# Performance work log

Measured on AMD Instinct MI355X. Metric: run time of the kernel, lower is better.

Reference implementation:

```python
import jax, jax.numpy as jnp
import numpy as np

N = 100_000      # nodes
E = 1_600_000    # edges (avg degree 16)
IN, H, OUT = 960, 192, 3
NB = 6           # block_num


def setup_inputs() -> dict:
    key = jax.random.key(0)
    ks = jax.random.split(key, 14)
    s = 0.05  # weight init scale
    x = jax.random.normal(ks[0], (N, IN), jnp.float32)
    src = jax.random.randint(ks[1], (E,), 0, N, jnp.int32)
    dst = jax.random.randint(ks[2], (E,), 0, N, jnp.int32)
    # normalized adjacency values (like D^-1 A entries)
    ew = jax.random.uniform(ks[3], (E,), jnp.float32) / 16.0
    w1 = jax.random.normal(ks[4], (IN, H), jnp.float32) * s
    l1 = jax.random.normal(ks[5], (IN, H), jnp.float32) * s
    b1 = jnp.zeros((H,), jnp.float32)
    wb = jax.random.normal(ks[6], (2 * NB, H, H), jnp.float32) * s
    lb = jax.random.normal(ks[7], (2 * NB, H, H), jnp.float32) * s
    bb = jnp.zeros((2 * NB, H), jnp.float32)
    w2 = jax.random.normal(ks[8], (H, OUT), jnp.float32) * s
    l2 = jax.random.normal(ks[9], (H, OUT), jnp.float32) * s
    b2 = jnp.zeros((OUT,), jnp.float32)
    return dict(x=x, src=src, dst=dst, ew=ew, w1=w1, l1=l1, b1=b1,
                wb=wb, lb=lb, bb=bb, w2=w2, l2=l2, b2=b2)


def reference(x, src, dst, ew, w1, l1, b1, wb, lb, bb, w2, l2, b2):
    def gcn(h, w, lw, b):
        # GraphConvolution: spmm(adj, h @ w) + h @ loop_w + b
        sup = h @ w                                   # [N, F_out]
        msg = sup[src] * ew[:, None]                  # gather + weight  [E, F_out]
        agg = jax.ops.segment_sum(msg, dst, num_segments=N)
        return agg + h @ lw + b

    h = gcn(x, w1, l1, b1)                            # conv1: in_dim -> hidden
    for i in range(NB):                               # GResBlocks
        a = gcn(h, wb[2 * i], lb[2 * i], bb[2 * i])
        a = gcn(a, wb[2 * i + 1], lb[2 * i + 1], bb[2 * i + 1])
        h = (h + a) * 0.5                             # residual scaling
    x_cat = h
    x_out = gcn(x_cat, w2, l2, b2)                    # conv2: hidden -> out_dim
    return (x_out, x_cat)
```

## Files before the change

### kernel.cpp

```cpp
#include <hip/hip_runtime.h>

typedef __attribute__((ext_vector_type(8))) short short8;
typedef __attribute__((ext_vector_type(4))) float f32x4;
typedef __attribute__((ext_vector_type(4))) int int4v;
typedef __attribute__((ext_vector_type(2))) unsigned int u32x2;

__device__ __forceinline__ float bf2f(unsigned short u) {
  return __uint_as_float(((unsigned)u) << 16);
}
__device__ __forceinline__ unsigned short f2bf(float f) {
  unsigned u = __float_as_uint(f);
  return (unsigned short)((u + 0x7FFFu + ((u >> 16) & 1u)) >> 16);
}

#define GLB_CAST(p) ((const __attribute__((address_space(1))) void*)(p))
#define LDS_CAST(p) ((__attribute__((address_space(3))) void*)(p))

__global__ void count_kernel(const int* __restrict__ dst, int* __restrict__ cnt, int E) {
  int e = blockIdx.x * blockDim.x + threadIdx.x;
  if (e < E) atomicAdd(&cnt[dst[e] + 1], 1);
}

__global__ __launch_bounds__(256) void scan_bsum_kernel(const int* __restrict__ cnt,
                                                        int* __restrict__ bsum, int n) {
  __shared__ int buf[256];
  int tid = threadIdx.x;
  int j0 = blockIdx.x * 1024 + tid * 4;
  int s = 0;
#pragma unroll
  for (int k = 0; k < 4; k++) {
    int j = j0 + k;
    if (j < n) s += cnt[j];
  }
  buf[tid] = s;
  __syncthreads();
  for (int off = 128; off > 0; off >>= 1) {
    if (tid < off) buf[tid] += buf[tid + off];
    __syncthreads();
  }
  if (tid == 0) bsum[blockIdx.x] = buf[0];
}

__global__ __launch_bounds__(256) void scan_small_kernel(const int* __restrict__ bsum,
                                                         int* __restrict__ boff, int nb) {
  __shared__ int buf[2][256];
  int tid = threadIdx.x;
  int C = (nb + 255) >> 8;
  int start = tid * C;
  int end = start + C; if (end > nb) end = nb;
  int s = 0;
  for (int j = start; j < end; j++) s += bsum[j];
  buf[0][tid] = s;
  __syncthreads();
  int pin = 0;
  for (int off = 1; off < 256; off <<= 1) {
    int v = buf[pin][tid];
    if (tid >= off) v += buf[pin][tid - off];
    buf[pin ^ 1][tid] = v;
    pin ^= 1;
    __syncthreads();
  }
  int run = (tid == 0) ? 0 : buf[pin][tid - 1];
  for (int j = start; j < end; j++) {
    boff[j] = run;
    run += bsum[j];
  }
}

__global__ __launch_bounds__(256) void scan_final_kernel(const int* __restrict__ cnt,
                                                         const int* __restrict__ boff,
                                                         int* __restrict__ rowptr,
                                                         int* __restrict__ cur,
                                                         int n, int nrows) {
  __shared__ int buf[2][256];
  int tid = threadIdx.x;
  int j0 = blockIdx.x * 1024 + tid * 4;
  int v[4];
  int s = 0;
#pragma unroll
  for (int k = 0; k < 4; k++) {
    int j = j0 + k;
    v[k] = (j < n) ? cnt[j] : 0;
    s += v[k];
  }
  buf[0][tid] = s;
  __syncthreads();
  int pin = 0;
  for (int off = 1; off < 256; off <<= 1) {
    int t = buf[pin][tid];
    if (tid >= off) t += buf[pin][tid - off];
    buf[pin ^ 1][tid] = t;
    pin ^= 1;
    __syncthreads();
  }
  int run = boff[blockIdx.x] + ((tid == 0) ? 0 : buf[pin][tid - 1]);
#pragma unroll
  for (int k = 0; k < 4; k++) {
    int j = j0 + k;
    if (j < n) {
      run += v[k];
      rowptr[j] = run;
      if (j < nrows) cur[j] = run;
    }
  }
}

__global__ void fill_kernel(const int* __restrict__ src, const int* __restrict__ dst,
                            const float* __restrict__ ew,
                            int* __restrict__ cur, int2* __restrict__ s_edge, int E) {
  int e = blockIdx.x * blockDim.x + threadIdx.x;
  if (e >= E) return;
  int r = dst[e];
  int pos = atomicAdd(&cur[r], 1);
  s_edge[pos] = make_int2(src[e], __float_as_int(ew[e]));
}

__global__ void prep_w_kernel(const float* __restrict__ w1,
                              const float* __restrict__ l1,
                              const float* __restrict__ wb,
                              const float* __restrict__ lb,
                              unsigned short* __restrict__ Wt1,
                              unsigned short* __restrict__ Wtb) {
  int tid = blockIdx.x * blockDim.x + threadIdx.x;
  const int n1 = 384 * 960;
  const int nb = 12 * 384 * 192;
  if (tid < n1) {
    int c = tid / 960, k = tid % 960;
    Wt1[tid] = f2bf((c < 192) ? w1[k * 192 + c] : l1[k * 192 + (c - 192)]);
  } else if (tid < n1 + nb) {
    int u = tid - n1;
    int i = u / (384 * 192);
    int r = u % (384 * 192);
    int c = r / 192, k = r % 192;
    Wtb[u] = f2bf((c < 192) ? wb[(i * 192 + k) * 192 + c]
                            : lb[(i * 192 + k) * 192 + (c - 192)]);
  }
}

__device__ __forceinline__ short8 cvt_f32x8(const float* p) {
  f32x4 a = *reinterpret_cast<const f32x4*>(p);
  f32x4 b = *reinterpret_cast<const f32x4*>(p + 4);
  short8 r;
  r[0] = (short)f2bf(a[0]); r[1] = (short)f2bf(a[1]);
  r[2] = (short)f2bf(a[2]); r[3] = (short)f2bf(a[3]);
  r[4] = (short)f2bf(b[0]); r[5] = (short)f2bf(b[1]);
  r[6] = (short)f2bf(b[2]); r[7] = (short)f2bf(b[3]);
  return r;
}

template <typename T>
__global__ __launch_bounds__(512) void gemm_kernel(const T* __restrict__ A,
                                                   const unsigned short* __restrict__ Wt,
                                                   unsigned short* __restrict__ out,
                                                   int nrows, int K) {
  __shared__ char lds_raw[40960];

  int tid = threadIdx.x;
  int lane = tid & 63;
  int w = tid >> 6;
  int rg = w >> 1, ch = w & 1;
  int row0blk = blockIdx.x * 256;
  int row0 = row0blk + rg * 64;
  int l15 = lane & 15, lq = lane >> 4;

  f32x4 acc[12][4];
#pragma unroll
  for (int cf = 0; cf < 12; cf++)
#pragma unroll
    for (int rf = 0; rf < 4; rf++) acc[cf][rf] = (f32x4)(0.0f);

  int tiles = K / 32;
  for (int tile = 0; tile < tiles; ++tile) {
    __syncthreads();
#pragma unroll
    for (int it = 0; it < 3; ++it) {
      int slot = it * 512 + tid;
      int q = slot / 384, c = slot - q * 384;
      const unsigned short* g = Wt + (size_t)c * K + tile * 32 + q * 8;
      __builtin_amdgcn_global_load_lds(GLB_CAST(g), LDS_CAST(lds_raw + 16384 + slot * 16), 16, 0, 0);
    }
#pragma unroll
    for (int it = 0; it < 2; ++it) {
      int slot = it * 512 + tid;
      int c = slot >> 8, row = slot & 255;
      int grow = row0blk + row;
      if (grow > nrows - 1) grow = nrows - 1;
      if constexpr (sizeof(T) == 2) {
        const T* g = A + (size_t)grow * K + tile * 32 + c * 8;
        __builtin_amdgcn_global_load_lds(GLB_CAST(g), LDS_CAST(lds_raw + slot * 16), 16, 0, 0);
      } else {
        const float* g = (const float*)A + (size_t)grow * K + tile * 32 + c * 8;
        *reinterpret_cast<short8*>(lds_raw + slot * 16) = cvt_f32x8(g);
      }
    }
    __syncthreads();

    short8 af[4];
#pragma unroll
    for (int rf = 0; rf < 4; rf++)
      af[rf] = *reinterpret_cast<const short8*>(
          lds_raw + lq * 4096 + (rg * 64 + rf * 16 + l15) * 16);
#pragma unroll
    for (int cf = 0; cf < 12; cf++) {
      const short8 bf = *reinterpret_cast<const short8*>(
          lds_raw + 16384 + (lq * 384 + ch * 192 + cf * 16 + l15) * 16);
#pragma unroll
      for (int rf = 0; rf < 4; rf++)
        acc[cf][rf] = __builtin_amdgcn_mfma_f32_16x16x32_bf16(bf, af[rf], acc[cf][rf], 0, 0, 0);
    }
  }

#pragma unroll
  for (int rf = 0; rf < 4; rf++) {
    int row = row0 + rf * 16 + l15;
    if (row >= nrows) continue;
    unsigned short* orow = out + (size_t)row * 384 + ch * 192 + lq * 4;
#pragma unroll
    for (int cf = 0; cf < 12; cf++) {
      u32x2 pv;
      pv[0] = (unsigned)f2bf(acc[cf][rf][0]) | ((unsigned)f2bf(acc[cf][rf][1]) << 16);
      pv[1] = (unsigned)f2bf(acc[cf][rf][2]) | ((unsigned)f2bf(acc[cf][rf][3]) << 16);
      *reinterpret_cast<u32x2*>(orow + cf * 16) = pv;
    }
  }
}

__global__ __launch_bounds__(256) void spmm_kernel(const unsigned short* __restrict__ t,
                                                   const int* __restrict__ rowptr,
                                                   const int2* __restrict__ s_edge,
                                                   const float* __restrict__ bias,
                                                   const float* __restrict__ hprev32,
                                                   unsigned short* __restrict__ out16,
                                                   float* __restrict__ out32,
                                                   int n, int mode) {
  int tid = blockIdx.x * blockDim.x + threadIdx.x;
  int node = tid / 24;
  int c = tid % 24;
  if (node >= n) return;

  float acc[8];
#pragma unroll
  for (int j = 0; j < 8; j++) acc[j] = 0.0f;

  int e0 = rowptr[node], e1 = rowptr[node + 1];
  int e = e0;
  for (; e + 4 <= e1; e += 4) {
    int2 ra = s_edge[e];
    int2 rb = s_edge[e + 1];
    int2 rc = s_edge[e + 2];
    int2 rd = s_edge[e + 3];
    float wa = __int_as_float(ra.y), wb = __int_as_float(rb.y);
    float wc = __int_as_float(rc.y), wd = __int_as_float(rd.y);
    short8 va = *reinterpret_cast<const short8*>(&t[(size_t)ra.x * 384 + c * 8]);
    short8 vb = *reinterpret_cast<const short8*>(&t[(size_t)rb.x * 384 + c * 8]);
    short8 vc = *reinterpret_cast<const short8*>(&t[(size_t)rc.x * 384 + c * 8]);
    short8 vd = *reinterpret_cast<const short8*>(&t[(size_t)rd.x * 384 + c * 8]);
#pragma unroll
    for (int j = 0; j < 8; j++) {
      acc[j] += wa * bf2f((unsigned short)va[j]) + wb * bf2f((unsigned short)vb[j]) +
                wc * bf2f((unsigned short)vc[j]) + wd * bf2f((unsigned short)vd[j]);
    }
  }
  for (; e < e1; e++) {
    int2 ra = s_edge[e];
    float wa = __int_as_float(ra.y);
    short8 va = *reinterpret_cast<const short8*>(&t[(size_t)ra.x * 384 + c * 8]);
#pragma unroll
    for (int j = 0; j < 8; j++) acc[j] += wa * bf2f((unsigned short)va[j]);
  }

  short8 hlv = *reinterpret_cast<const short8*>(&t[(size_t)node * 384 + 192 + c * 8]);
  float r[8];
#pragma unroll
  for (int j = 0; j < 8; j++)
    r[j] = acc[j] + bf2f((unsigned short)hlv[j]) + bias[c * 8 + j];

  if (mode == 1) {
#pragma unroll
    for (int j = 0; j < 8; j++)
      r[j] = 0.5f * (hprev32[(size_t)node * 192 + c * 8 + j] + r[j]);
  }

  unsigned short o16[8];
#pragma unroll
  for (int j = 0; j < 8; j++) o16[j] = f2bf(r[j]);
  *reinterpret_cast<int4v*>(&out16[(size_t)node * 192 + c * 8]) =
      *reinterpret_cast<const int4v*>(o16);

  if (out32) {
    f32x4 lo, hi;
    lo[0] = r[0]; lo[1] = r[1]; lo[2] = r[2]; lo[3] = r[3];
    hi[0] = r[4]; hi[1] = r[5]; hi[2] = r[6]; hi[3] = r[7];
    *reinterpret_cast<f32x4*>(&out32[(size_t)node * 192 + c * 8]) = lo;
    *reinterpret_cast<f32x4*>(&out32[(size_t)node * 192 + c * 8 + 4]) = hi;
  }
}

__global__ __launch_bounds__(256) void conv2a_kernel(const float* __restrict__ h,
                                                     const float* __restrict__ w2,
                                                     const float* __restrict__ l2,
                                                     const float* __restrict__ b2,
                                                     float* __restrict__ sup2,
                                                     float* __restrict__ hl2, int n) {
  int wid = (blockIdx.x * blockDim.x + threadIdx.x) >> 6;
  int lane = threadIdx.x & 63;
  if (wid >= n) return;
  float sa[3] = {0.f, 0.f, 0.f}, sl[3] = {0.f, 0.f, 0.f};
  for (int k = lane; k < 192; k += 64) {
    float hv = h[(size_t)wid * 192 + k];
#pragma unroll
    for (int j = 0; j < 3; j++) {
      sa[j] += hv * w2[k * 3 + j];
      sl[j] += hv * l2[k * 3 + j];
    }
  }
#pragma unroll
  for (int j = 0; j < 3; j++) {
    for (int off = 32; off > 0; off >>= 1) {
      sa[j] += __shfl_down(sa[j], off);
      sl[j] += __shfl_down(sl[j], off);
    }
  }
  if (lane == 0) {
#pragma unroll
    for (int j = 0; j < 3; j++) {
      sup2[(size_t)wid * 3 + j] = sa[j];
      hl2[(size_t)wid * 3 + j] = sl[j] + b2[j];
    }
  }
}

__global__ __launch_bounds__(256) void conv2b_kernel(const int* __restrict__ rowptr,
                                                     const int2* __restrict__ s_edge,
                                                     const float* __restrict__ sup2,
                                                     const float* __restrict__ hl2,
                                                     float* __restrict__ out, int n) {
  int node = blockIdx.x * blockDim.x + threadIdx.x;
  if (node >= n) return;
  float acc[3] = {0.f, 0.f, 0.f};
  int e0 = rowptr[node], e1 = rowptr[node + 1];
  for (int e = e0; e < e1; e++) {
    int2 rec = s_edge[e];
    float wgt = __int_as_float(rec.y);
#pragma unroll
    for (int j = 0; j < 3; j++) acc[j] += wgt * sup2[(size_t)rec.x * 3 + j];
  }
#pragma unroll
  for (int j = 0; j < 3; j++)
    out[(size_t)node * 3 + j] = acc[j] + hl2[(size_t)node * 3 + j];
}

extern "C" void kernel_launch(void* const* d_in, const int* in_sizes, int n_in,
                              void* d_out, int out_size, void* d_ws, size_t ws_size,
                              hipStream_t stream) {
  const float* x  = (const float*)d_in[0];
  const int* src  = (const int*)d_in[1];
  const int* dst  = (const int*)d_in[2];
  const float* ew = (const float*)d_in[3];
  const float* w1 = (const float*)d_in[4];
  const float* l1 = (const float*)d_in[5];
  const float* b1 = (const float*)d_in[6];
  const float* wb = (const float*)d_in[7];
  const float* lb = (const float*)d_in[8];
  const float* bb = (const float*)d_in[9];
  const float* w2 = (const float*)d_in[10];
  const float* l2 = (const float*)d_in[11];
  const float* b2 = (const float*)d_in[12];
  float* out = (float*)d_out;

  const int N = in_sizes[0] / 960;
  const int E = in_sizes[1];

  float* h32 = out + (size_t)N * 3;

  char* p = (char*)d_ws;
  auto alloc = [&](size_t bytes) {
    char* q = p;
    p += (bytes + 255) & ~(size_t)255;
    return q;
  };
  unsigned short* Wt1 = (unsigned short*)alloc((size_t)384 * 960 * 2);
  unsigned short* Wtb = (unsigned short*)alloc((size_t)12 * 384 * 192 * 2);
  unsigned short* t   = (unsigned short*)alloc((size_t)N * 384 * 2);
  unsigned short* h16 = (unsigned short*)alloc((size_t)N * 192 * 2);
  unsigned short* a16 = (unsigned short*)alloc((size_t)N * 192 * 2);
  int* rowptr = (int*)alloc((size_t)(N + 1) * 4);
  int* cur    = (int*)alloc((size_t)N * 4);
  int* cnt    = (int*)alloc((size_t)(N + 1) * 4);
  int* bsum   = (int*)alloc((size_t)1024 * 4);
  int* boff   = (int*)alloc((size_t)1024 * 4);
  int2* s_edge = (int2*)alloc((size_t)E * 8);
  float* sup2 = (float*)alloc((size_t)N * 3 * 4);
  float* hl2  = (float*)alloc((size_t)N * 3 * 4);
  if ((size_t)(p - (char*)d_ws) > ws_size) return;

  const int nScan = N + 1;
  const int nBlk = (nScan + 1023) / 1024;

  hipMemsetAsync(cnt, 0, (size_t)(N + 1) * 4, stream);
  count_kernel<<<(E + 255) / 256, 256, 0, stream>>>(dst, cnt, E);
  scan_bsum_kernel<<<nBlk, 256, 0, stream>>>(cnt, bsum, nScan);
  scan_small_kernel<<<1, 256, 0, stream>>>(bsum, boff, nBlk);
  scan_final_kernel<<<nBlk, 256, 0, stream>>>(cnt, boff, rowptr, cur, nScan, N);
  fill_kernel<<<(E + 255) / 256, 256, 0, stream>>>(src, dst, ew, cur, s_edge, E);
  {
    int total = 384 * 960 + 12 * 384 * 192;
    prep_w_kernel<<<(total + 255) / 256, 256, 0, stream>>>(w1, l1, wb, lb, Wt1, Wtb);
  }

  int gBlocks = (N + 255) / 256;
  int sBlocks = (N * 24 + 255) / 256;

  gemm_kernel<float><<<gBlocks, 512, 0, stream>>>(x, Wt1, t, N, 960);
  spmm_kernel<<<sBlocks, 256, 0, stream>>>(t, rowptr, s_edge, b1,
                                           (const float*)nullptr, h16, h32, N, 0);

  for (int i = 0; i < 12; i += 2) {
    gemm_kernel<unsigned short><<<gBlocks, 512, 0, stream>>>(
        h16, Wtb + (size_t)i * 384 * 192, t, N, 192);
    spmm_kernel<<<sBlocks, 256, 0, stream>>>(t, rowptr, s_edge, bb + (size_t)i * 192,
                                             (const float*)nullptr, a16, (float*)nullptr, N, 0);
    gemm_kernel<unsigned short><<<gBlocks, 512, 0, stream>>>(
        a16, Wtb + (size_t)(i + 1) * 384 * 192, t, N, 192);
    spmm_kernel<<<sBlocks, 256, 0, stream>>>(t, rowptr, s_edge, bb + (size_t)(i + 1) * 192,
                                             h32, h16, h32, N, 1);
  }

  conv2a_kernel<<<(N + 3) / 4, 256, 0, stream>>>(h32, w2, l2, b2, sup2, hl2, N);
  conv2b_kernel<<<(N + 255) / 256, 256, 0, stream>>>(rowptr, s_edge, sup2, hl2, out, N);
}
```

Before: 2.569 ms.

## Double-buffer bf16 GEMM LDS staging and unroll SpMM gather to 8 edges

Splits the templated GEMM into an fp32-input kernel and a bf16 kernel that double-buffers its tiles in 80 KB of dynamic LDS. The next tile's global_load_lds is issued before the MFMA work on the current tile, so loads overlap compute and one barrier per tile is removed. The SpMM inner loop now gathers 8 neighbour rows per iteration instead of 4, giving more loads in flight. In exchange, the larger LDS footprint lowers how many GEMM blocks fit on a CU, and the longer SpMM unroll raises register pressure.

```diff
diff --git a/kernel.cpp b/kernel.cpp
--- a/kernel.cpp
+++ b/kernel.cpp
@@ -148,11 +148,10 @@
   return r;
 }
 
-template <typename T>
-__global__ __launch_bounds__(512) void gemm_kernel(const T* __restrict__ A,
-                                                   const unsigned short* __restrict__ Wt,
-                                                   unsigned short* __restrict__ out,
-                                                   int nrows, int K) {
+__global__ __launch_bounds__(512) void gemm_f32_kernel(const float* __restrict__ A,
+                                                       const unsigned short* __restrict__ Wt,
+                                                       unsigned short* __restrict__ out,
+                                                       int nrows, int K) {
   __shared__ char lds_raw[40960];
 
   int tid = threadIdx.x;
@@ -185,13 +184,8 @@
       int c = slot >> 8, row = slot & 255;
       int grow = row0blk + row;
       if (grow > nrows - 1) grow = nrows - 1;
-      if constexpr (sizeof(T) == 2) {
-        const T* g = A + (size_t)grow * K + tile * 32 + c * 8;
-        __builtin_amdgcn_global_load_lds(GLB_CAST(g), LDS_CAST(lds_raw + slot * 16), 16, 0, 0);
-      } else {
-        const float* g = (const float*)A + (size_t)grow * K + tile * 32 + c * 8;
-        *reinterpret_cast<short8*>(lds_raw + slot * 16) = cvt_f32x8(g);
-      }
+      const float* g = A + (size_t)grow * K + tile * 32 + c * 8;
+      *reinterpret_cast<short8*>(lds_raw + slot * 16) = cvt_f32x8(g);
     }
     __syncthreads();
 
@@ -208,6 +202,85 @@
       for (int rf = 0; rf < 4; rf++)
         acc[cf][rf] = __builtin_amdgcn_mfma_f32_16x16x32_bf16(bf, af[rf], acc[cf][rf], 0, 0, 0);
     }
+  }
+
+#pragma unroll
+  for (int rf = 0; rf < 4; rf++) {
+    int row = row0 + rf * 16 + l15;
+    if (row >= nrows) continue;
+    unsigned short* orow = out + (size_t)row * 384 + ch * 192 + lq * 4;
+#pragma unroll
+    for (int cf = 0; cf < 12; cf++) {
+      u32x2 pv;
+      pv[0] = (unsigned)f2bf(acc[cf][rf][0]) | ((unsigned)f2bf(acc[cf][rf][1]) << 16);
+      pv[1] = (unsigned)f2bf(acc[cf][rf][2]) | ((unsigned)f2bf(acc[cf][rf][3]) << 16);
+      *reinterpret_cast<u32x2*>(orow + cf * 16) = pv;
+    }
+  }
+}
+
+__global__ __launch_bounds__(512) void gemm_bf16_db_kernel(const unsigned short* __restrict__ A,
+                                                           const unsigned short* __restrict__ Wt,
+                                                           unsigned short* __restrict__ out,
+                                                           int nrows, int K) {
+  extern __shared__ char lds_db[];
+
+  int tid = threadIdx.x;
+  int lane = tid & 63;
+  int w = tid >> 6;
+  int rg = w >> 1, ch = w & 1;
+  int row0blk = blockIdx.x * 256;
+  int row0 = row0blk + rg * 64;
+  int l15 = lane & 15, lq = lane >> 4;
+
+  f32x4 acc[12][4];
+#pragma unroll
+  for (int cf = 0; cf < 12; cf++)
+#pragma unroll
+    for (int rf = 0; rf < 4; rf++) acc[cf][rf] = (f32x4)(0.0f);
+
+  auto stage = [&](int tile, int buf) {
+    char* base = lds_db + buf * 40960;
+#pragma unroll
+    for (int it = 0; it < 3; ++it) {
+      int slot = it * 512 + tid;
+      int q = slot / 384, c = slot - q * 384;
+      const unsigned short* g = Wt + (size_t)c * K + tile * 32 + q * 8;
+      __builtin_amdgcn_global_load_lds(GLB_CAST(g), LDS_CAST(base + 16384 + slot * 16), 16, 0, 0);
+    }
+#pragma unroll
+    for (int it = 0; it < 2; ++it) {
+      int slot = it * 512 + tid;
+      int c = slot >> 8, row = slot & 255;
+      int grow = row0blk + row;
+      if (grow > nrows - 1) grow = nrows - 1;
+      const unsigned short* g = A + (size_t)grow * K + tile * 32 + c * 8;
+      __builtin_amdgcn_global_load_lds(GLB_CAST(g), LDS_CAST(base + slot * 16), 16, 0, 0);
+    }
+  };
+
+  int tiles = K / 32;
+  stage(0, 0);
+  __syncthreads();
+  int cur = 0;
+  for (int tile = 0; tile < tiles; ++tile) {
+    if (tile + 1 < tiles) stage(tile + 1, cur ^ 1);
+    char* base = lds_db + cur * 40960;
+    short8 af[4];
+#pragma unroll
+    for (int rf = 0; rf < 4; rf++)
+      af[rf] = *reinterpret_cast<const short8*>(
+          base + lq * 4096 + (rg * 64 + rf * 16 + l15) * 16);
+#pragma unroll
+    for (int cf = 0; cf < 12; cf++) {
+      const short8 bf = *reinterpret_cast<const short8*>(
+          base + 16384 + (lq * 384 + ch * 192 + cf * 16 + l15) * 16);
+#pragma unroll
+      for (int rf = 0; rf < 4; rf++)
+        acc[cf][rf] = __builtin_amdgcn_mfma_f32_16x16x32_bf16(bf, af[rf], acc[cf][rf], 0, 0, 0);
+    }
+    __syncthreads();
+    cur ^= 1;
   }
 
 #pragma unroll
@@ -244,24 +317,32 @@
 
   int e0 = rowptr[node], e1 = rowptr[node + 1];
   int e = e0;
-  for (; e + 4 <= e1; e += 4) {
+  for (; e + 8 <= e1; e += 8) {
+    int2 rec[8];
+#pragma unroll
+    for (int k = 0; k < 8; k++) rec[k] = s_edge[e + k];
+    short8 v[8];
+#pragma unroll
+    for (int k = 0; k < 8; k++)
+      v[k] = *reinterpret_cast<const short8*>(&t[(size_t)rec[k].x * 384 + c * 8]);
+#pragma unroll
+    for (int k = 0; k < 8; k++) {
+      float wgt = __int_as_float(rec[k].y);
+#pragma unroll
+      for (int j = 0; j < 8; j++) acc[j] += wgt * bf2f((unsigned short)v[k][j]);
+    }
+  }
+  for (; e + 2 <= e1; e += 2) {
     int2 ra = s_edge[e];
     int2 rb = s_edge[e + 1];
-    int2 rc = s_edge[e + 2];
-    int2 rd = s_edge[e + 3];
     float wa = __int_as_float(ra.y), wb = __int_as_float(rb.y);
-    float wc = __int_as_float(rc.y), wd = __int_as_float(rd.y);
     short8 va = *reinterpret_cast<const short8*>(&t[(size_t)ra.x * 384 + c * 8]);
     short8 vb = *reinterpret_cast<const short8*>(&t[(size_t)rb.x * 384 + c * 8]);
-    short8 vc = *reinterpret_cast<const short8*>(&t[(size_t)rc.x * 384 + c * 8]);
-    short8 vd = *reinterpret_cast<const short8*>(&t[(size_t)rd.x * 384 + c * 8]);
-#pragma unroll
-    for (int j = 0; j < 8; j++) {
-      acc[j] += wa * bf2f((unsigned short)va[j]) + wb * bf2f((unsigned short)vb[j]) +
-                wc * bf2f((unsigned short)vc[j]) + wd * bf2f((unsigned short)vd[j]);
-    }
-  }
-  for (; e < e1; e++) {
+#pragma unroll
+    for (int j = 0; j < 8; j++)
+      acc[j] += wa * bf2f((unsigned short)va[j]) + wb * bf2f((unsigned short)vb[j]);
+  }
+  if (e < e1) {
     int2 ra = s_edge[e];
     float wa = __int_as_float(ra.y);
     short8 va = *reinterpret_cast<const short8*>(&t[(size_t)ra.x * 384 + c * 8]);
@@ -410,17 +491,18 @@
 
   int gBlocks = (N + 255) / 256;
   int sBlocks = (N * 24 + 255) / 256;
-
-  gemm_kernel<float><<<gBlocks, 512, 0, stream>>>(x, Wt1, t, N, 960);
+  const int DB_LDS = 81920;
+
+  gemm_f32_kernel<<<gBlocks, 512, 0, stream>>>(x, Wt1, t, N, 960);
   spmm_kernel<<<sBlocks, 256, 0, stream>>>(t, rowptr, s_edge, b1,
                                            (const float*)nullptr, h16, h32, N, 0);
 
   for (int i = 0; i < 12; i += 2) {
-    gemm_kernel<unsigned short><<<gBlocks, 512, 0, stream>>>(
+    gemm_bf16_db_kernel<<<gBlocks, 512, DB_LDS, stream>>>(
         h16, Wtb + (size_t)i * 384 * 192, t, N, 192);
     spmm_kernel<<<sBlocks, 256, 0, stream>>>(t, rowptr, s_edge, bb + (size_t)i * 192,
                                              (const float*)nullptr, a16, (float*)nullptr, N, 0);
-    gemm_kernel<unsigned short><<<gBlocks, 512, 0, stream>>>(
+    gemm_bf16_db_kernel<<<gBlocks, 512, DB_LDS, stream>>>(
         a16, Wtb + (size_t)(i + 1) * 384 * 192, t, N, 192);
     spmm_kernel<<<sBlocks, 256, 0, stream>>>(t, rowptr, s_edge, bb + (size_t)(i + 1) * 192,
                                              h32, h16, h32, N, 1);
```

After: 2.528 ms. About the same (-1.6%).

## Double-buffer GEMM LDS tiles with 128-row blocks and widen SpMM per-thread columns

Applied to the files above, without the earlier changes.

The GEMM kernel is rewritten to double-buffer LDS, prefetching the next K tile of A and weights while MFMAs run on the current one. The row tile shrinks from 256 to 128 rows per block, and the fp32 input conversion is deferred until after compute. The SpMM kernel now handles 16 columns per thread instead of 8, using 12 threads per node. The aim is to hide global-load latency in the GEMM and cut redundant edge-record loads in SpMM, at the cost of more registers and lower occupancy (64KB dynamic LDS per block).

```diff
diff --git a/kernel.cpp b/kernel.cpp
--- a/kernel.cpp
+++ b/kernel.cpp
@@ -137,9 +137,7 @@
   }
 }
 
-__device__ __forceinline__ short8 cvt_f32x8(const float* p) {
-  f32x4 a = *reinterpret_cast<const f32x4*>(p);
-  f32x4 b = *reinterpret_cast<const f32x4*>(p + 4);
+__device__ __forceinline__ short8 cvt_pair(f32x4 a, f32x4 b) {
   short8 r;
   r[0] = (short)f2bf(a[0]); r[1] = (short)f2bf(a[1]);
   r[2] = (short)f2bf(a[2]); r[3] = (short)f2bf(a[3]);
@@ -149,70 +147,96 @@
 }
 
 template <typename T>
-__global__ __launch_bounds__(512) void gemm_kernel(const T* __restrict__ A,
-                                                   const unsigned short* __restrict__ Wt,
-                                                   unsigned short* __restrict__ out,
-                                                   int nrows, int K) {
-  __shared__ char lds_raw[40960];
+__global__ __launch_bounds__(512) void gemm_db_kernel(const T* __restrict__ A,
+                                                      const unsigned short* __restrict__ Wt,
+                                                      unsigned short* __restrict__ out,
+                                                      int nrows, int K) {
+  extern __shared__ char lds[];
+  const int BUF = 32768;
 
   int tid = threadIdx.x;
   int lane = tid & 63;
   int w = tid >> 6;
   int rg = w >> 1, ch = w & 1;
-  int row0blk = blockIdx.x * 256;
-  int row0 = row0blk + rg * 64;
+  int row0blk = blockIdx.x * 128;
   int l15 = lane & 15, lq = lane >> 4;
 
-  f32x4 acc[12][4];
-#pragma unroll
-  for (int cf = 0; cf < 12; cf++)
-#pragma unroll
-    for (int rf = 0; rf < 4; rf++) acc[cf][rf] = (f32x4)(0.0f);
-
-  int tiles = K / 32;
-  for (int tile = 0; tile < tiles; ++tile) {
-    __syncthreads();
+  int skq = tid >> 7, srow = tid & 127;
+  int sgrow = row0blk + srow;
+  if (sgrow > nrows - 1) sgrow = nrows - 1;
+
+  f32x4 acc[12][2];
+#pragma unroll
+  for (int cf = 0; cf < 12; cf++) {
+    acc[cf][0] = (f32x4)(0.0f);
+    acc[cf][1] = (f32x4)(0.0f);
+  }
+
+  auto stageB = [&](int tile, int buf) {
 #pragma unroll
     for (int it = 0; it < 3; ++it) {
       int slot = it * 512 + tid;
       int q = slot / 384, c = slot - q * 384;
       const unsigned short* g = Wt + (size_t)c * K + tile * 32 + q * 8;
-      __builtin_amdgcn_global_load_lds(GLB_CAST(g), LDS_CAST(lds_raw + 16384 + slot * 16), 16, 0, 0);
-    }
-#pragma unroll
-    for (int it = 0; it < 2; ++it) {
-      int slot = it * 512 + tid;
-      int c = slot >> 8, row = slot & 255;
-      int grow = row0blk + row;
-      if (grow > nrows - 1) grow = nrows - 1;
+      __builtin_amdgcn_global_load_lds(GLB_CAST(g), LDS_CAST(lds + buf * BUF + 8192 + slot * 16),
+                                       16, 0, 0);
+    }
+  };
+
+  int tiles = K / 32;
+  stageB(0, 0);
+  if constexpr (sizeof(T) == 2) {
+    const T* g = A + (size_t)sgrow * K + skq * 8;
+    __builtin_amdgcn_global_load_lds(GLB_CAST(g), LDS_CAST(lds + tid * 16), 16, 0, 0);
+  } else {
+    const float* g = (const float*)A + (size_t)sgrow * K + skq * 8;
+    f32x4 a0 = *reinterpret_cast<const f32x4*>(g);
+    f32x4 a1 = *reinterpret_cast<const f32x4*>(g + 4);
+    *reinterpret_cast<short8*>(lds + tid * 16) = cvt_pair(a0, a1);
+  }
+  __syncthreads();
+
+  int cur = 0;
+  for (int tile = 0; tile < tiles; ++tile) {
+    bool pf = (tile + 1 < tiles);
+    f32x4 a0, a1;
+    if (pf) {
+      stageB(tile + 1, cur ^ 1);
       if constexpr (sizeof(T) == 2) {
-        const T* g = A + (size_t)grow * K + tile * 32 + c * 8;
-        __builtin_amdgcn_global_load_lds(GLB_CAST(g), LDS_CAST(lds_raw + slot * 16), 16, 0, 0);
+        const T* g = A + (size_t)sgrow * K + (tile + 1) * 32 + skq * 8;
+        __builtin_amdgcn_global_load_lds(GLB_CAST(g), LDS_CAST(lds + (cur ^ 1) * BUF + tid * 16),
+                                         16, 0, 0);
       } else {
-        const float* g = (const float*)A + (size_t)grow * K + tile * 32 + c * 8;
-        *reinterpret_cast<short8*>(lds_raw + slot * 16) = cvt_f32x8(g);
+        const float* g = (const float*)A + (size_t)sgrow * K + (tile + 1) * 32 + skq * 8;
+        a0 = *reinterpret_cast<const f32x4*>(g);
+        a1 = *reinterpret_cast<const f32x4*>(g + 4);
       }
     }
-    __syncthreads();
-
-    short8 af[4];
-#pragma unroll
-    for (int rf = 0; rf < 4; rf++)
-      af[rf] = *reinterpret_cast<const short8*>(
-          lds_raw + lq * 4096 + (rg * 64 + rf * 16 + l15) * 16);
+
+    char* base = lds + cur * BUF;
+    short8 af[2];
+#pragma unroll
+    for (int rf = 0; rf < 2; rf++)
+      af[rf] = *reinterpret_cast<const short8*>(base + (lq * 128 + rg * 32 + rf * 16 + l15) * 16);
 #pragma unroll
     for (int cf = 0; cf < 12; cf++) {
       const short8 bf = *reinterpret_cast<const short8*>(
-          lds_raw + 16384 + (lq * 384 + ch * 192 + cf * 16 + l15) * 16);
-#pragma unroll
-      for (int rf = 0; rf < 4; rf++)
-        acc[cf][rf] = __builtin_amdgcn_mfma_f32_16x16x32_bf16(bf, af[rf], acc[cf][rf], 0, 0, 0);
-    }
-  }
-
-#pragma unroll
-  for (int rf = 0; rf < 4; rf++) {
-    int row = row0 + rf * 16 + l15;
+          base + 8192 + (lq * 384 + ch * 192 + cf * 16 + l15) * 16);
+      acc[cf][0] = __builtin_amdgcn_mfma_f32_16x16x32_bf16(bf, af[0], acc[cf][0], 0, 0, 0);
+      acc[cf][1] = __builtin_amdgcn_mfma_f32_16x16x32_bf16(bf, af[1], acc[cf][1], 0, 0, 0);
+    }
+
+    if constexpr (sizeof(T) == 4) {
+      if (pf)
+        *reinterpret_cast<short8*>(lds + (cur ^ 1) * BUF + tid * 16) = cvt_pair(a0, a1);
+    }
+    __syncthreads();
+    cur ^= 1;
+  }
+
+#pragma unroll
+  for (int rf = 0; rf < 2; rf++) {
+    int row = row0blk + rg * 32 + rf * 16 + l15;
     if (row >= nrows) continue;
     unsigned short* orow = out + (size_t)row * 384 + ch * 192 + lq * 4;
 #pragma unroll
@@ -234,65 +258,81 @@
                                                    float* __restrict__ out32,
                                                    int n, int mode) {
   int tid = blockIdx.x * blockDim.x + threadIdx.x;
-  int node = tid / 24;
-  int c = tid % 24;
+  int node = tid / 12;
+  int c = tid % 12;
   if (node >= n) return;
 
-  float acc[8];
-#pragma unroll
-  for (int j = 0; j < 8; j++) acc[j] = 0.0f;
+  float acc[16];
+#pragma unroll
+  for (int j = 0; j < 16; j++) acc[j] = 0.0f;
 
   int e0 = rowptr[node], e1 = rowptr[node + 1];
   int e = e0;
   for (; e + 4 <= e1; e += 4) {
-    int2 ra = s_edge[e];
-    int2 rb = s_edge[e + 1];
-    int2 rc = s_edge[e + 2];
-    int2 rd = s_edge[e + 3];
-    float wa = __int_as_float(ra.y), wb = __int_as_float(rb.y);
-    float wc = __int_as_float(rc.y), wd = __int_as_float(rd.y);
-    short8 va = *reinterpret_cast<const short8*>(&t[(size_t)ra.x * 384 + c * 8]);
-    short8 vb = *reinterpret_cast<const short8*>(&t[(size_t)rb.x * 384 + c * 8]);
-    short8 vc = *reinterpret_cast<const short8*>(&t[(size_t)rc.x * 384 + c * 8]);
-    short8 vd = *reinterpret_cast<const short8*>(&t[(size_t)rd.x * 384 + c * 8]);
-#pragma unroll
-    for (int j = 0; j < 8; j++) {
-      acc[j] += wa * bf2f((unsigned short)va[j]) + wb * bf2f((unsigned short)vb[j]) +
-                wc * bf2f((unsigned short)vc[j]) + wd * bf2f((unsigned short)vd[j]);
+    int2 rec[4];
+#pragma unroll
+    for (int k = 0; k < 4; k++) rec[k] = s_edge[e + k];
+    short8 v0[4], v1[4];
+#pragma unroll
+    for (int k = 0; k < 4; k++) {
+      const unsigned short* row = &t[(size_t)rec[k].x * 384 + c * 16];
+      v0[k] = *reinterpret_cast<const short8*>(row);
+      v1[k] = *reinterpret_cast<const short8*>(row + 8);
+    }
+#pragma unroll
+    for (int k = 0; k < 4; k++) {
+      float wgt = __int_as_float(rec[k].y);
+#pragma unroll
+      for (int j = 0; j < 8; j++) {
+        acc[j] += wgt * bf2f((unsigned short)v0[k][j]);
+        acc[8 + j] += wgt * bf2f((unsigned short)v1[k][j]);
+      }
     }
   }
   for (; e < e1; e++) {
     int2 ra = s_edge[e];
     float wa = __int_as_float(ra.y);
-    short8 va = *reinterpret_cast<const short8*>(&t[(size_t)ra.x * 384 + c * 8]);
-#pragma unroll
-    for (int j = 0; j < 8; j++) acc[j] += wa * bf2f((unsigned short)va[j]);
-  }
-
-  short8 hlv = *reinterpret_cast<const short8*>(&t[(size_t)node * 384 + 192 + c * 8]);
-  float r[8];
-#pragma unroll
-  for (int j = 0; j < 8; j++)
-    r[j] = acc[j] + bf2f((unsigned short)hlv[j]) + bias[c * 8 + j];
+    const unsigned short* row = &t[(size_t)ra.x * 384 + c * 16];
+    short8 v0 = *reinterpret_cast<const short8*>(row);
+    short8 v1 = *reinterpret_cast<const short8*>(row + 8);
+#pragma unroll
+    for (int j = 0; j < 8; j++) {
+      acc[j] += wa * bf2f((unsigned short)v0[j]);
+      acc[8 + j] += wa * bf2f((unsigned short)v1[j]);
+    }
+  }
+
+  const unsigned short* hlrow = &t[(size_t)node * 384 + 192 + c * 16];
+  short8 hl0 = *reinterpret_cast<const short8*>(hlrow);
+  short8 hl1 = *reinterpret_cast<const short8*>(hlrow + 8);
+  float r[16];
+#pragma unroll
+  for (int j = 0; j < 8; j++) {
+    r[j] = acc[j] + bf2f((unsigned short)hl0[j]) + bias[c * 16 + j];
+    r[8 + j] = acc[8 + j] + bf2f((unsigned short)hl1[j]) + bias[c * 16 + 8 + j];
+  }
 
   if (mode == 1) {
 #pragma unroll
-    for (int j = 0; j < 8; j++)
-      r[j] = 0.5f * (hprev32[(size_t)node * 192 + c * 8 + j] + r[j]);
-  }
-
-  unsigned short o16[8];
-#pragma unroll
-  for (int j = 0; j < 8; j++) o16[j] = f2bf(r[j]);
-  *reinterpret_cast<int4v*>(&out16[(size_t)node * 192 + c * 8]) =
-      *reinterpret_cast<const int4v*>(o16);
+    for (int j = 0; j < 16; j++)
+      r[j] = 0.5f * (hprev32[(size_t)node * 192 + c * 16 + j] + r[j]);
+  }
+
+  unsigned short o16[16];
+#pragma unroll
+  for (int j = 0; j < 16; j++) o16[j] = f2bf(r[j]);
+  int4v* odst = reinterpret_cast<int4v*>(&out16[(size_t)node * 192 + c * 16]);
+  odst[0] = reinterpret_cast<const int4v*>(o16)[0];
+  odst[1] = reinterpret_cast<const int4v*>(o16)[1];
 
   if (out32) {
-    f32x4 lo, hi;
-    lo[0] = r[0]; lo[1] = r[1]; lo[2] = r[2]; lo[3] = r[3];
-    hi[0] = r[4]; hi[1] = r[5]; hi[2] = r[6]; hi[3] = r[7];
-    *reinterpret_cast<f32x4*>(&out32[(size_t)node * 192 + c * 8]) = lo;
-    *reinterpret_cast<f32x4*>(&out32[(size_t)node * 192 + c * 8 + 4]) = hi;
+    float* wdst = &out32[(size_t)node * 192 + c * 16];
+#pragma unroll
+    for (int q = 0; q < 4; q++) {
+      f32x4 v;
+      v[0] = r[q * 4 + 0]; v[1] = r[q * 4 + 1]; v[2] = r[q * 4 + 2]; v[3] = r[q * 4 + 3];
+      *reinterpret_cast<f32x4*>(wdst + q * 4) = v;
+    }
   }
 }
 
@@ -408,19 +448,20 @@
     prep_w_kernel<<<(total + 255) / 256, 256, 0, stream>>>(w1, l1, wb, lb, Wt1, Wtb);
   }
 
-  int gBlocks = (N + 255) / 256;
-  int sBlocks = (N * 24 + 255) / 256;
-
-  gemm_kernel<float><<<gBlocks, 512, 0, stream>>>(x, Wt1, t, N, 960);
+  int gBlocks = (N + 127) / 128;
+  int sBlocks = (N * 12 + 255) / 256;
+  const int DB_LDS = 65536;
+
+  gemm_db_kernel<float><<<gBlocks, 512, DB_LDS, stream>>>(x, Wt1, t, N, 960);
   spmm_kernel<<<sBlocks, 256, 0, stream>>>(t, rowptr, s_edge, b1,
                                            (const float*)nullptr, h16, h32, N, 0);
 
   for (int i = 0; i < 12; i += 2) {
-    gemm_kernel<unsigned short><<<gBlocks, 512, 0, stream>>>(
+    gemm_db_kernel<unsigned short><<<gBlocks, 512, DB_LDS, stream>>>(
         h16, Wtb + (size_t)i * 384 * 192, t, N, 192);
     spmm_kernel<<<sBlocks, 256, 0, stream>>>(t, rowptr, s_edge, bb + (size_t)i * 192,
                                              (const float*)nullptr, a16, (float*)nullptr, N, 0);
-    gemm_kernel<unsigned short><<<gBlocks, 512, 0, stream>>>(
+    gemm_db_kernel<unsigned short><<<gBlocks, 512, DB_LDS, stream>>>(
         a16, Wtb + (size_t)(i + 1) * 384 * 192, t, N, 192);
     spmm_kernel<<<sBlocks, 256, 0, stream>>>(t, rowptr, s_edge, bb + (size_t)(i + 1) * 192,
                                              h32, h16, h32, N, 1);
```

Result: slower. 2.645 ms (+3.0%).

## Double-buffer GEMM LDS tiles with smaller blocks and unroll SpMM gather by eight

Applied to the files above, without the earlier changes.

The GEMM now uses 256-thread blocks, each computing a 128-row by 192-column tile, with two LDS buffers. The next K tile is prefetched while MFMAs run on the current one, and fp32 input conversion is deferred until after compute. This is meant to hide global-load latency and remove one barrier per tile, at the cost of doubling the number of blocks and reloading the A rows for each column half. The SpMM inner loop now issues eight independent gathers per iteration instead of four, for more memory-level parallelism, at the cost of extra register pressure.

```diff
diff --git a/kernel.cpp b/kernel.cpp
--- a/kernel.cpp
+++ b/kernel.cpp
@@ -137,9 +137,7 @@
   }
 }
 
-__device__ __forceinline__ short8 cvt_f32x8(const float* p) {
-  f32x4 a = *reinterpret_cast<const f32x4*>(p);
-  f32x4 b = *reinterpret_cast<const f32x4*>(p + 4);
+__device__ __forceinline__ short8 cvt_pair(f32x4 a, f32x4 b) {
   short8 r;
   r[0] = (short)f2bf(a[0]); r[1] = (short)f2bf(a[1]);
   r[2] = (short)f2bf(a[2]); r[3] = (short)f2bf(a[3]);
@@ -149,72 +147,120 @@
 }
 
 template <typename T>
-__global__ __launch_bounds__(512) void gemm_kernel(const T* __restrict__ A,
-                                                   const unsigned short* __restrict__ Wt,
-                                                   unsigned short* __restrict__ out,
-                                                   int nrows, int K) {
-  __shared__ char lds_raw[40960];
+__global__ __launch_bounds__(256, 4) void gemm_db_kernel(const T* __restrict__ A,
+                                                         const unsigned short* __restrict__ Wt,
+                                                         unsigned short* __restrict__ out,
+                                                         int nrows, int K) {
+  extern __shared__ char lds[];
+  const int BUF = 20480;
 
   int tid = threadIdx.x;
   int lane = tid & 63;
-  int w = tid >> 6;
-  int rg = w >> 1, ch = w & 1;
-  int row0blk = blockIdx.x * 256;
-  int row0 = row0blk + rg * 64;
+  int rg = tid >> 6;
+  int row0blk = (blockIdx.x >> 1) * 128;
+  int cbase = (blockIdx.x & 1) * 192;
   int l15 = lane & 15, lq = lane >> 4;
 
-  f32x4 acc[12][4];
-#pragma unroll
-  for (int cf = 0; cf < 12; cf++)
-#pragma unroll
-    for (int rf = 0; rf < 4; rf++) acc[cf][rf] = (f32x4)(0.0f);
+  int srow = tid & 127;
+  int sgrow = row0blk + srow;
+  if (sgrow > nrows - 1) sgrow = nrows - 1;
+
+  f32x4 acc[12][2];
+#pragma unroll
+  for (int cf = 0; cf < 12; cf++) {
+    acc[cf][0] = (f32x4)(0.0f);
+    acc[cf][1] = (f32x4)(0.0f);
+  }
+
+  auto stageB = [&](int tile, int buf) {
+#pragma unroll
+    for (int it = 0; it < 3; ++it) {
+      int slot = it * 256 + tid;
+      int q = slot / 192, c = slot - q * 192;
+      const unsigned short* g = Wt + (size_t)(cbase + c) * K + tile * 32 + q * 8;
+      __builtin_amdgcn_global_load_lds(GLB_CAST(g), LDS_CAST(lds + buf * BUF + 8192 + slot * 16),
+                                       16, 0, 0);
+    }
+  };
+  auto stageA16 = [&](int tile, int buf) {
+#pragma unroll
+    for (int it = 0; it < 2; ++it) {
+      int slot = it * 256 + tid;
+      int q = slot >> 7;
+      const unsigned short* g = (const unsigned short*)A + (size_t)sgrow * K + tile * 32 + q * 8;
+      __builtin_amdgcn_global_load_lds(GLB_CAST(g), LDS_CAST(lds + buf * BUF + slot * 16), 16, 0, 0);
+    }
+  };
 
   int tiles = K / 32;
+  stageB(0, 0);
+  if constexpr (sizeof(T) == 2) {
+    stageA16(0, 0);
+  } else {
+#pragma unroll
+    for (int it = 0; it < 2; ++it) {
+      int slot = it * 256 + tid;
+      int q = slot >> 7;
+      const float* g = (const float*)A + (size_t)sgrow * K + q * 8;
+      f32x4 a0 = *reinterpret_cast<const f32x4*>(g);
+      f32x4 a1 = *reinterpret_cast<const f32x4*>(g + 4);
+      *reinterpret_cast<short8*>(lds + slot * 16) = cvt_pair(a0, a1);
+    }
+  }
+  __syncthreads();
+
+  int cur = 0;
   for (int tile = 0; tile < tiles; ++tile) {
-    __syncthreads();
-#pragma unroll
-    for (int it = 0; it < 3; ++it) {
-      int slot = it * 512 + tid;
-      int q = slot / 384, c = slot - q * 384;
-      const unsigned short* g = Wt + (size_t)c * K + tile * 32 + q * 8;
-      __builtin_amdgcn_global_load_lds(GLB_CAST(g), LDS_CAST(lds_raw + 16384 + slot * 16), 16, 0, 0);
-    }
-#pragma unroll
-    for (int it = 0; it < 2; ++it) {
-      int slot = it * 512 + tid;
-      int c = slot >> 8, row = slot & 255;
-      int grow = row0blk + row;
-      if (grow > nrows - 1) grow = nrows - 1;
+    bool pf = (tile + 1 < tiles);
+    f32x4 pa[4];
+    if (pf) {
+      stageB(tile + 1, cur ^ 1);
       if constexpr (sizeof(T) == 2) {
-        const T* g = A + (size_t)grow * K + tile * 32 + c * 8;
-        __builtin_amdgcn_global_load_lds(GLB_CAST(g), LDS_CAST(lds_raw + slot * 16), 16, 0, 0);
+        stageA16(tile + 1, cur ^ 1);
       } else {
-        const float* g = (const float*)A + (size_t)grow * K + tile * 32 + c * 8;
-        *reinterpret_cast<short8*>(lds_raw + slot * 16) = cvt_f32x8(g);
+#pragma unroll
+        for (int it = 0; it < 2; ++it) {
+          int slot = it * 256 + tid;
+          int q = slot >> 7;
+          const float* g = (const float*)A + (size_t)sgrow * K + (tile + 1) * 32 + q * 8;
+          pa[it * 2] = *reinterpret_cast<const f32x4*>(g);
+          pa[it * 2 + 1] = *reinterpret_cast<const f32x4*>(g + 4);
+        }
       }
     }
-    __syncthreads();
-
-    short8 af[4];
-#pragma unroll
-    for (int rf = 0; rf < 4; rf++)
-      af[rf] = *reinterpret_cast<const short8*>(
-          lds_raw + lq * 4096 + (rg * 64 + rf * 16 + l15) * 16);
+
+    char* base = lds + cur * BUF;
+    short8 af[2];
+#pragma unroll
+    for (int rf = 0; rf < 2; rf++)
+      af[rf] = *reinterpret_cast<const short8*>(base + (lq * 128 + rg * 32 + rf * 16 + l15) * 16);
 #pragma unroll
     for (int cf = 0; cf < 12; cf++) {
       const short8 bf = *reinterpret_cast<const short8*>(
-          lds_raw + 16384 + (lq * 384 + ch * 192 + cf * 16 + l15) * 16);
-#pragma unroll
-      for (int rf = 0; rf < 4; rf++)
-        acc[cf][rf] = __builtin_amdgcn_mfma_f32_16x16x32_bf16(bf, af[rf], acc[cf][rf], 0, 0, 0);
-    }
-  }
-
-#pragma unroll
-  for (int rf = 0; rf < 4; rf++) {
-    int row = row0 + rf * 16 + l15;
+          base + 8192 + (lq * 192 + cf * 16 + l15) * 16);
+      acc[cf][0] = __builtin_amdgcn_mfma_f32_16x16x32_bf16(bf, af[0], acc[cf][0], 0, 0, 0);
+      acc[cf][1] = __builtin_amdgcn_mfma_f32_16x16x32_bf16(bf, af[1], acc[cf][1], 0, 0, 0);
+    }
+
+    if constexpr (sizeof(T) == 4) {
+      if (pf) {
+        char* nbase = lds + (cur ^ 1) * BUF;
+#pragma unroll
+        for (int it = 0; it < 2; ++it) {
+          int slot = it * 256 + tid;
+          *reinterpret_cast<short8*>(nbase + slot * 16) = cvt_pair(pa[it * 2], pa[it * 2 + 1]);
+        }
+      }
+    }
+    __syncthreads();
+    cur ^= 1;
+  }
+
+#pragma unroll
+  for (int rf = 0; rf < 2; rf++) {
+    int row = row0blk + rg * 32 + rf * 16 + l15;
     if (row >= nrows) continue;
-    unsigned short* orow = out + (size_t)row * 384 + ch * 192 + lq * 4;
+    unsigned short* orow = out + (size_t)row * 384 + cbase + lq * 4;
 #pragma unroll
     for (int cf = 0; cf < 12; cf++) {
       u32x2 pv;
@@ -244,24 +290,32 @@
 
   int e0 = rowptr[node], e1 = rowptr[node + 1];
   int e = e0;
-  for (; e + 4 <= e1; e += 4) {
+  for (; e + 8 <= e1; e += 8) {
+    int2 rec[8];
+#pragma unroll
+    for (int k = 0; k < 8; k++) rec[k] = s_edge[e + k];
+    short8 v[8];
+#pragma unroll
+    for (int k = 0; k < 8; k++)
+      v[k] = *reinterpret_cast<const short8*>(&t[(size_t)rec[k].x * 384 + c * 8]);
+#pragma unroll
+    for (int k = 0; k < 8; k++) {
+      float wgt = __int_as_float(rec[k].y);
+#pragma unroll
+      for (int j = 0; j < 8; j++) acc[j] += wgt * bf2f((unsigned short)v[k][j]);
+    }
+  }
+  for (; e + 2 <= e1; e += 2) {
     int2 ra = s_edge[e];
     int2 rb = s_edge[e + 1];
-    int2 rc = s_edge[e + 2];
-    int2 rd = s_edge[e + 3];
     float wa = __int_as_float(ra.y), wb = __int_as_float(rb.y);
-    float wc = __int_as_float(rc.y), wd = __int_as_float(rd.y);
     short8 va = *reinterpret_cast<const short8*>(&t[(size_t)ra.x * 384 + c * 8]);
     short8 vb = *reinterpret_cast<const short8*>(&t[(size_t)rb.x * 384 + c * 8]);
-    short8 vc = *reinterpret_cast<const short8*>(&t[(size_t)rc.x * 384 + c * 8]);
-    short8 vd = *reinterpret_cast<const short8*>(&t[(size_t)rd.x * 384 + c * 8]);
-#pragma unroll
-    for (int j = 0; j < 8; j++) {
-      acc[j] += wa * bf2f((unsigned short)va[j]) + wb * bf2f((unsigned short)vb[j]) +
-                wc * bf2f((unsigned short)vc[j]) + wd * bf2f((unsigned short)vd[j]);
-    }
-  }
-  for (; e < e1; e++) {
+#pragma unroll
+    for (int j = 0; j < 8; j++)
+      acc[j] += wa * bf2f((unsigned short)va[j]) + wb * bf2f((unsigned short)vb[j]);
+  }
+  if (e < e1) {
     int2 ra = s_edge[e];
     float wa = __int_as_float(ra.y);
     short8 va = *reinterpret_cast<const short8*>(&t[(size_t)ra.x * 384 + c * 8]);
@@ -408,19 +462,20 @@
     prep_w_kernel<<<(total + 255) / 256, 256, 0, stream>>>(w1, l1, wb, lb, Wt1, Wtb);
   }
 
-  int gBlocks = (N + 255) / 256;
+  int gBlocks = ((N + 127) / 128) * 2;
   int sBlocks = (N * 24 + 255) / 256;
-
-  gemm_kernel<float><<<gBlocks, 512, 0, stream>>>(x, Wt1, t, N, 960);
+  const int DB_LDS = 40960;
+
+  gemm_db_kernel<float><<<gBlocks, 256, DB_LDS, stream>>>(x, Wt1, t, N, 960);
   spmm_kernel<<<sBlocks, 256, 0, stream>>>(t, rowptr, s_edge, b1,
                                            (const float*)nullptr, h16, h32, N, 0);
 
   for (int i = 0; i < 12; i += 2) {
-    gemm_kernel<unsigned short><<<gBlocks, 512, 0, stream>>>(
+    gemm_db_kernel<unsigned short><<<gBlocks, 256, DB_LDS, stream>>>(
         h16, Wtb + (size_t)i * 384 * 192, t, N, 192);
     spmm_kernel<<<sBlocks, 256, 0, stream>>>(t, rowptr, s_edge, bb + (size_t)i * 192,
                                              (const float*)nullptr, a16, (float*)nullptr, N, 0);
-    gemm_kernel<unsigned short><<<gBlocks, 512, 0, stream>>>(
+    gemm_db_kernel<unsigned short><<<gBlocks, 256, DB_LDS, stream>>>(
         a16, Wtb + (size_t)(i + 1) * 384 * 192, t, N, 192);
     spmm_kernel<<<sBlocks, 256, 0, stream>>>(t, rowptr, s_edge, bb + (size_t)(i + 1) * 192,
                                              h32, h16, h32, N, 1);
```

Result: slower. 2.622 ms (+2.0%).
